# Kernel optimization log

Measured on AMD Instinct MI355X. Metric: run time of the kernel, lower is better.

The kernel has to match this reference:

```python
import jax, jax.numpy as jnp
import numpy as np

G_N, G_K, G_R = 1024, 32, 0.2
BN_EPS = 1e-5


def fps(p, n_sample):
    """Furthest point sampling. p: [B,N,3] -> idx [B,n_sample] int32."""
    B, N, _ = p.shape

    def step(carry, _):
        dist, last = carry  # dist [B,N], last [B]
        lp = jnp.take_along_axis(p, last[:, None, None], axis=1)  # [B,1,3]
        d = jnp.sum((p - lp) ** 2, axis=-1)  # [B,N]
        dist = jnp.minimum(dist, d)
        nxt = jnp.argmax(dist, axis=1).astype(jnp.int32)
        return (dist, nxt), last

    init = (jnp.full((B, N), 1e10, p.dtype), jnp.zeros((B,), jnp.int32))
    _, idx = jax.lax.scan(step, init, None, length=n_sample)
    return idx.T  # [B, n_sample]


def ball_query(p, q, k, r):
    """p: [B,N,3], q: [B,S,3] -> [B,S,k] int32 neighbor indices (pad with first)."""
    B, N, _ = p.shape
    sq = jnp.sum((q[:, :, None, :] - p[:, None, :, :]) ** 2, axis=-1)  # [B,S,N]
    idx = jnp.where(sq <= r * r, jnp.arange(N, dtype=jnp.int32)[None, None, :], N)
    idx = jnp.sort(idx, axis=-1)[..., :k]  # first k in-ball indices (by index order)
    first = idx[..., :1]
    return jnp.where(idx == N, first, idx).astype(jnp.int32)


def gather_group(x, idx):
    """x: [B,N,C], idx: [B,S,K] -> [B,S,K,C]."""
    B, S, K = idx.shape
    C = x.shape[-1]
    flat = jnp.take_along_axis(x, idx.reshape(B, S * K, 1), axis=1)
    return flat.reshape(B, S, K, C)


def mlp_bn_relu(x, W, b, gamma, beta):
    """1x1 conv + BatchNorm (batch stats) + ReLU on [B,S,K,Cin]."""
    x = jnp.einsum('bskc,cd->bskd', x, W) + b
    m = jnp.mean(x, axis=(0, 1, 2))
    v = jnp.var(x, axis=(0, 1, 2))
    x = (x - m) * jax.lax.rsqrt(v + BN_EPS) * gamma + beta
    return jax.nn.relu(x)


def setup_inputs() -> dict:
    key = jax.random.key(0)
    ks = jax.random.split(key, 8)
    B, N, C = 16, 4096, 64
    d_feats = [64, 64, 128]
    inp = {
        'f': jax.random.normal(ks[0], (B, N, C), dtype=jnp.float32),
        'p': jax.random.uniform(ks[1], (B, N, 3), dtype=jnp.float32),
    }
    d_in = C + 3
    for i, d_out in enumerate(d_feats):
        inp[f'W{i}'] = jax.random.normal(ks[2 + i], (d_in, d_out), dtype=jnp.float32) * 0.05
        inp[f'b{i}'] = jnp.zeros((d_out,), jnp.float32)
        inp[f'gamma{i}'] = jnp.ones((d_out,), jnp.float32)
        inp[f'beta{i}'] = jnp.zeros((d_out,), jnp.float32)
        d_in = d_out
    return inp


def reference(f, p, W0, b0, gamma0, beta0, W1, b1, gamma1, beta1, W2, b2, gamma2, beta2):
    qry_idx = fps(p, G_N)                                   # [B,S]
    qry_pnt = jnp.take_along_axis(p, qry_idx[..., None], axis=1)  # [B,S,3]
    grp_idx = ball_query(p, qry_pnt, G_K, G_R)              # [B,S,K]
    grp_pnt = gather_group(p, grp_idx) - qry_pnt[:, :, None, :]   # [B,S,K,3]
    grp_fea = jnp.concatenate([gather_group(f, grp_idx), grp_pnt], axis=-1)  # [B,S,K,C+3]
    x = mlp_bn_relu(grp_fea, W0, b0, gamma0, beta0)
    x = mlp_bn_relu(x, W1, b1, gamma1, beta1)
    x = mlp_bn_relu(x, W2, b2, gamma2, beta2)
    f_out = jnp.max(x, axis=2)  # max-pool over neighborhood -> [B,S,128]
    return (f_out, qry_pnt)
```

## Files before the change

kernel.cpp:

```cpp
#include <hip/hip_runtime.h>

#define NB 16
#define NP 4096
#define CF 64
#define NS 1024
#define NK 32
#define NROWS (NB*NS*NK)

typedef float f32x4 __attribute__((ext_vector_type(4)));
typedef __bf16 bf16x8 __attribute__((ext_vector_type(8)));
typedef unsigned short u16x8 __attribute__((ext_vector_type(8)));

__device__ __forceinline__ unsigned short f2bf(float f){
  unsigned u = __float_as_uint(f);
  return (unsigned short)((u + 0x7FFFu + ((u>>16)&1u)) >> 16);
}
__device__ __forceinline__ float bf2f(unsigned short s){
  return __uint_as_float(((unsigned)s)<<16);
}

__device__ __forceinline__ float dppmax_b1(float x){
  int y=__builtin_amdgcn_update_dpp(0,__float_as_int(x),0xB1,0xF,0xF,true);
  return fmaxf(x,__int_as_float(y));
}
__device__ __forceinline__ float dppmax_4e(float x){
  int y=__builtin_amdgcn_update_dpp(0,__float_as_int(x),0x4E,0xF,0xF,true);
  return fmaxf(x,__int_as_float(y));
}
__device__ __forceinline__ float dppmax_hm(float x){
  int y=__builtin_amdgcn_update_dpp(0,__float_as_int(x),0x141,0xF,0xF,true);
  return fmaxf(x,__int_as_float(y));
}
__device__ __forceinline__ float dppmax_m(float x){
  int y=__builtin_amdgcn_update_dpp(0,__float_as_int(x),0x140,0xF,0xF,true);
  return fmaxf(x,__int_as_float(y));
}

#define FPS_T 256
#define FPS_PT (NP/FPS_T)
__global__ __launch_bounds__(FPS_T) void fps_kernel(const float* __restrict__ p,
                                                    float* __restrict__ qry){
  __shared__ float4 P4[NP];
  __shared__ unsigned long long warr[2][4];
  const int b = blockIdx.x, tid = threadIdx.x;
  const int lane = tid & 63, wid = tid >> 6;
  const float* pb = p + (size_t)b*NP*3;
  float px[FPS_PT], py[FPS_PT], pz[FPS_PT], dist[FPS_PT];
#pragma unroll
  for (int g=0; g<4; g++){
    const int i0 = tid*FPS_PT + g*4;
    const float* src = pb + (size_t)i0*3;
    f32x4 a = *(const f32x4*)(src);
    f32x4 c = *(const f32x4*)(src+4);
    f32x4 d = *(const f32x4*)(src+8);
    px[g*4+0]=a[0]; py[g*4+0]=a[1]; pz[g*4+0]=a[2];
    px[g*4+1]=a[3]; py[g*4+1]=c[0]; pz[g*4+1]=c[1];
    px[g*4+2]=c[2]; py[g*4+2]=c[3]; pz[g*4+2]=d[0];
    px[g*4+3]=d[1]; py[g*4+3]=d[2]; pz[g*4+3]=d[3];
#pragma unroll
    for (int j=0;j<4;j++){
      P4[i0+j]=make_float4(px[g*4+j],py[g*4+j],pz[g*4+j],0.f);
      dist[g*4+j]=1e10f;
    }
  }
  __syncthreads();
  float4 lp0 = P4[0];
  float lx=lp0.x, ly=lp0.y, lz=lp0.z;
  for (int t=0;t<NS;t++){
    if (tid==0){
      size_t o=(size_t)(b*NS+t)*3;
      qry[o+0]=lx; qry[o+1]=ly; qry[o+2]=lz;
    }
    float bv=-1.0f; int bi=0;
#pragma unroll
    for (int j=0;j<FPS_PT;j++){
      float dx=__fsub_rn(px[j],lx), dy=__fsub_rn(py[j],ly), dz=__fsub_rn(pz[j],lz);
      float d=__fadd_rn(__fadd_rn(__fmul_rn(dx,dx),__fmul_rn(dy,dy)),__fmul_rn(dz,dz));
      dist[j]=fminf(dist[j],d);
      if (dist[j]>bv){ bv=dist[j]; bi=j; }
    }
    const int gbi = tid*FPS_PT + bi;
    float m = bv;
    m = dppmax_b1(m);
    m = dppmax_4e(m);
    m = dppmax_hm(m);
    m = dppmax_m(m);
    unsigned m0 = (unsigned)__builtin_amdgcn_readlane(__float_as_int(m), 0);
    unsigned m1 = (unsigned)__builtin_amdgcn_readlane(__float_as_int(m), 16);
    unsigned m2 = (unsigned)__builtin_amdgcn_readlane(__float_as_int(m), 32);
    unsigned m3 = (unsigned)__builtin_amdgcn_readlane(__float_as_int(m), 48);
    unsigned ma = m0>m1?m0:m1, mb = m2>m3?m2:m3;
    unsigned mu = ma>mb?ma:mb;
    unsigned long long ball = __ballot(__float_as_uint(bv)==mu);
    int srcl = (int)(__ffsll((long long)ball) - 1);
    int widx = __builtin_amdgcn_readlane(gbi, srcl);
    if (lane==0)
      warr[t&1][wid] = ((unsigned long long)mu<<32)
                     | (unsigned)(0xFFFFFFFFu-(unsigned)widx);
    __syncthreads();
    unsigned long long k0=warr[t&1][0], k1=warr[t&1][1],
                       k2=warr[t&1][2], k3=warr[t&1][3];
    unsigned long long ka = k0>k1?k0:k1, kb = k2>k3?k2:k3;
    unsigned long long bk = ka>kb?ka:kb;
    const int winner = (int)(0xFFFFFFFFu-(unsigned)(bk & 0xFFFFFFFFull));
    float4 lp = P4[winner];
    lx=lp.x; ly=lp.y; lz=lp.z;
  }
}

#define BQ_T 512
__global__ __launch_bounds__(BQ_T) void ballq_kernel(const float* __restrict__ p,
                                                     const float* __restrict__ qry,
                                                     int* __restrict__ grp){
  __shared__ float PX[NP], PY[NP], PZ[NP];
  const int tid = threadIdx.x, lane = tid & 63, w = tid >> 6;
  const int b  = blockIdx.x >> 7;
  const int s0 = (blockIdx.x & 127) * 8;
  const float* pb = p + (size_t)b*NP*3;
  for (int i = tid; i < NP; i += BQ_T){
    PX[i]=pb[i*3+0]; PY[i]=pb[i*3+1]; PZ[i]=pb[i*3+2];
  }
  __syncthreads();
  const int s = s0 + w;
  const float* q = qry + (size_t)(b*NS+s)*3;
  const float qx=q[0], qy=q[1], qz=q[2];
  int* out = grp + (size_t)(b*NS+s)*NK;
  const float RR = (float)(0.2*0.2);
  int cum = 0, first = 0;
  for (int j=0;j<NP/64;j++){
    const int idx = j*64 + lane;
    float dx=__fsub_rn(qx,PX[idx]), dy=__fsub_rn(qy,PY[idx]), dz=__fsub_rn(qz,PZ[idx]);
    float sq=__fadd_rn(__fadd_rn(__fmul_rn(dx,dx),__fmul_rn(dy,dy)),__fmul_rn(dz,dz));
    const bool in_r = (sq <= RR);
    unsigned long long ball = __ballot(in_r);
    if (ball){
      if (cum == 0) first = j*64 + (int)__builtin_ctzll(ball);
      int below = __builtin_amdgcn_mbcnt_hi((unsigned)(ball>>32),
                    __builtin_amdgcn_mbcnt_lo((unsigned)ball, 0));
      int pos = cum + below;
      if (in_r && pos < NK) out[pos] = idx;
      cum += (int)__popcll(ball);
      if (cum >= NK) break;
    }
  }
  const int cnt = cum < NK ? cum : NK;
  if (lane >= cnt && lane < NK) out[lane] = first;
}

__global__ void zero_slots_kernel(float* __restrict__ slots){
  int i = blockIdx.x*256 + threadIdx.x;
  if (i < 64*256) slots[i]=0.0f;
}

#define TPW 8
__global__ __launch_bounds__(256) void gemm0_kernel(const float* __restrict__ f,
    const float* __restrict__ p, const float* __restrict__ qry,
    const int* __restrict__ grp, const float* __restrict__ W0,
    const float* __restrict__ b0, unsigned short* __restrict__ ybuf,
    float* __restrict__ slots){
  const int tid=threadIdx.x, lane=tid&63, w=tid>>6;
  const int lg=lane>>4, lr=lane&15;
  bf16x8 bw[3][4];
#pragma unroll
  for (int kc=0;kc<3;kc++)
#pragma unroll
    for (int nt=0;nt<4;nt++){
      u16x8 t;
#pragma unroll
      for (int j=0;j<8;j++){
        int k = kc*32 + lg*8 + j, n = nt*16 + lr;
        float v = (k<67) ? W0[k*64+n] : 0.0f;
        t[j]=f2bf(v);
      }
      bw[kc][nt]=__builtin_bit_cast(bf16x8,t);
    }
  float bs[4];
#pragma unroll
  for (int nt=0;nt<4;nt++) bs[nt]=b0[nt*16+lr];
  float ssum[4]={0,0,0,0}, ssq[4]={0,0,0,0};
  const int base_row = blockIdx.x*512;
  const int b = base_row / (NS*NK);
  for (int ti=0;ti<TPW;ti++){
    const int R0 = base_row + (w*TPW+ti)*16;
    const int Ra = R0 + lr;
    const int idxp = grp[Ra];
    const float* frow = f + ((size_t)(b*NP+idxp))*64;
    f32x4 u0=*(const f32x4*)(frow + lg*8);
    f32x4 u1=*(const f32x4*)(frow + lg*8 + 4);
    f32x4 u2=*(const f32x4*)(frow + 32 + lg*8);
    f32x4 u3=*(const f32x4*)(frow + 36 + lg*8);
    u16x8 t0, t1;
#pragma unroll
    for (int j=0;j<4;j++){
      t0[j]=f2bf(u0[j]); t0[4+j]=f2bf(u1[j]);
      t1[j]=f2bf(u2[j]); t1[4+j]=f2bf(u3[j]);
    }
    u16x8 t2={0,0,0,0,0,0,0,0};
    if (lg==0){
      const int qidx = Ra >> 5;
      const float* pp = p + ((size_t)(b*NP+idxp))*3;
      const float* qq = qry + (size_t)qidx*3;
      t2[0]=f2bf(__fsub_rn(pp[0],qq[0]));
      t2[1]=f2bf(__fsub_rn(pp[1],qq[1]));
      t2[2]=f2bf(__fsub_rn(pp[2],qq[2]));
    }
    bf16x8 a0=__builtin_bit_cast(bf16x8,t0);
    bf16x8 a1=__builtin_bit_cast(bf16x8,t1);
    bf16x8 a2=__builtin_bit_cast(bf16x8,t2);
#pragma unroll
    for (int nt=0;nt<4;nt++){
      f32x4 acc={0,0,0,0};
      acc=__builtin_amdgcn_mfma_f32_16x16x32_bf16(a0,bw[0][nt],acc,0,0,0);
      acc=__builtin_amdgcn_mfma_f32_16x16x32_bf16(a1,bw[1][nt],acc,0,0,0);
      acc=__builtin_amdgcn_mfma_f32_16x16x32_bf16(a2,bw[2][nt],acc,0,0,0);
#pragma unroll
      for (int r=0;r<4;r++){
        float v = acc[r] + bs[nt];
        ssum[nt]+=v; ssq[nt]+=v*v;
        ybuf[(size_t)(R0 + lg*4 + r)*64 + nt*16 + lr] = f2bf(v);
      }
    }
  }
  float* slot = slots + (size_t)(blockIdx.x & 63)*256;
#pragma unroll
  for (int nt=0;nt<4;nt++){
    float s1=ssum[nt], s2=ssq[nt];
    s1 += __shfl_xor(s1,16); s1 += __shfl_xor(s1,32);
    s2 += __shfl_xor(s2,16); s2 += __shfl_xor(s2,32);
    if (lane<16){
      atomicAdd(slot + nt*16+lr, s1);
      atomicAdd(slot + 128 + nt*16+lr, s2);
    }
  }
}

__global__ void finalize_kernel(float* __restrict__ slots,
                                const float* __restrict__ gamma,
                                const float* __restrict__ beta,
                                float* __restrict__ par, int Cc){
  const int c = threadIdx.x;
  float s1=0.f, s2=0.f;
  for (int i=0;i<64;i++){ s1+=slots[i*256+c]; s2+=slots[i*256+128+c]; }
  const float invM = 1.0f/(float)NROWS;
  if (c<Cc){
    float mean = s1*invM;
    float var  = s2*invM - mean*mean;
    float scale = gamma[c]/sqrtf(var + 1e-5f);
    par[c]      = scale;
    par[128+c]  = beta[c] - mean*scale;
  }
  for (int i=0;i<64;i++){ slots[i*256+c]=0.f; slots[i*256+128+c]=0.f; }
}

__global__ __launch_bounds__(256) void gemm1_kernel(unsigned short* __restrict__ ybuf,
    const float* __restrict__ W, const float* __restrict__ bv,
    const float* __restrict__ par0, float* __restrict__ slots){
  const int tid=threadIdx.x, lane=tid&63, w=tid>>6;
  const int lg=lane>>4, lr=lane&15;
  float sc[2][8], sh[2][8];
#pragma unroll
  for (int kc=0;kc<2;kc++){
    int c0=kc*32+lg*8;
#pragma unroll
    for (int j=0;j<8;j++){ sc[kc][j]=par0[c0+j]; sh[kc][j]=par0[128+c0+j]; }
  }
  bf16x8 bw[2][4];
#pragma unroll
  for (int kc=0;kc<2;kc++)
#pragma unroll
    for (int nt=0;nt<4;nt++){
      u16x8 t;
#pragma unroll
      for (int j=0;j<8;j++){
        int k=kc*32+lg*8+j, n=nt*16+lr;
        t[j]=f2bf(W[k*64+n]);
      }
      bw[kc][nt]=__builtin_bit_cast(bf16x8,t);
    }
  float bs[4];
#pragma unroll
  for (int nt=0;nt<4;nt++) bs[nt]=bv[nt*16+lr];
  float ssum[4]={0,0,0,0}, ssq[4]={0,0,0,0};
  const int base_row = blockIdx.x*512;
  for (int ti=0;ti<TPW;ti++){
    const int R0 = base_row + (w*TPW+ti)*16;
    const unsigned short* yr = ybuf + (size_t)(R0+lr)*64;
    bf16x8 a[2];
#pragma unroll
    for (int kc=0;kc<2;kc++){
      u16x8 rv = *(const u16x8*)(yr + kc*32 + lg*8);
      u16x8 t;
#pragma unroll
      for (int j=0;j<8;j++){
        float v = bf2f(rv[j]);
        v = fmaxf(fmaf(v, sc[kc][j], sh[kc][j]), 0.f);
        t[j]=f2bf(v);
      }
      a[kc]=__builtin_bit_cast(bf16x8,t);
    }
#pragma unroll
    for (int nt=0;nt<4;nt++){
      f32x4 acc={0,0,0,0};
      acc=__builtin_amdgcn_mfma_f32_16x16x32_bf16(a[0],bw[0][nt],acc,0,0,0);
      acc=__builtin_amdgcn_mfma_f32_16x16x32_bf16(a[1],bw[1][nt],acc,0,0,0);
#pragma unroll
      for (int r=0;r<4;r++){
        float v = acc[r] + bs[nt];
        ssum[nt]+=v; ssq[nt]+=v*v;
        ybuf[(size_t)(R0 + lg*4 + r)*64 + nt*16 + lr] = f2bf(v);
      }
    }
  }
  float* slot = slots + (size_t)(blockIdx.x & 63)*256;
#pragma unroll
  for (int nt=0;nt<4;nt++){
    float s1=ssum[nt], s2=ssq[nt];
    s1 += __shfl_xor(s1,16); s1 += __shfl_xor(s1,32);
    s2 += __shfl_xor(s2,16); s2 += __shfl_xor(s2,32);
    if (lane<16){
      atomicAdd(slot + nt*16+lr, s1);
      atomicAdd(slot + 128 + nt*16+lr, s2);
    }
  }
}

__global__ __launch_bounds__(256) void gemm2stats_kernel(const unsigned short* __restrict__ ybuf,
    const float* __restrict__ W, const float* __restrict__ bv,
    const float* __restrict__ par1, float* __restrict__ slots){
  const int tid=threadIdx.x, lane=tid&63, w=tid>>6;
  const int lg=lane>>4, lr=lane&15;
  float sc[2][8], sh[2][8];
#pragma unroll
  for (int kc=0;kc<2;kc++){
    int c0=kc*32+lg*8;
#pragma unroll
    for (int j=0;j<8;j++){ sc[kc][j]=par1[c0+j]; sh[kc][j]=par1[128+c0+j]; }
  }
  bf16x8 bw[2][8];
#pragma unroll
  for (int kc=0;kc<2;kc++)
#pragma unroll
    for (int nt=0;nt<8;nt++){
      u16x8 t;
#pragma unroll
      for (int j=0;j<8;j++){
        int k=kc*32+lg*8+j, n=nt*16+lr;
        t[j]=f2bf(W[k*128+n]);
      }
      bw[kc][nt]=__builtin_bit_cast(bf16x8,t);
    }
  float bs[8], ssum[8], ssq[8];
#pragma unroll
  for (int nt=0;nt<8;nt++){ bs[nt]=bv[nt*16+lr]; ssum[nt]=0.f; ssq[nt]=0.f; }
  const int base_row = blockIdx.x*512;
  for (int ti=0;ti<TPW;ti++){
    const int R0 = base_row + (w*TPW+ti)*16;
    const unsigned short* yr = ybuf + (size_t)(R0+lr)*64;
    bf16x8 a[2];
#pragma unroll
    for (int kc=0;kc<2;kc++){
      u16x8 rv = *(const u16x8*)(yr + kc*32 + lg*8);
      u16x8 t;
#pragma unroll
      for (int j=0;j<8;j++){
        float v = bf2f(rv[j]);
        v = fmaxf(fmaf(v, sc[kc][j], sh[kc][j]), 0.f);
        t[j]=f2bf(v);
      }
      a[kc]=__builtin_bit_cast(bf16x8,t);
    }
#pragma unroll
    for (int nt=0;nt<8;nt++){
      f32x4 acc={0,0,0,0};
      acc=__builtin_amdgcn_mfma_f32_16x16x32_bf16(a[0],bw[0][nt],acc,0,0,0);
      acc=__builtin_amdgcn_mfma_f32_16x16x32_bf16(a[1],bw[1][nt],acc,0,0,0);
#pragma unroll
      for (int r=0;r<4;r++){
        float v = acc[r] + bs[nt];
        ssum[nt]+=v; ssq[nt]+=v*v;
      }
    }
  }
  float* slot = slots + (size_t)(blockIdx.x & 63)*256;
#pragma unroll
  for (int nt=0;nt<8;nt++){
    float s1=ssum[nt], s2=ssq[nt];
    s1 += __shfl_xor(s1,16); s1 += __shfl_xor(s1,32);
    s2 += __shfl_xor(s2,16); s2 += __shfl_xor(s2,32);
    if (lane<16){
      atomicAdd(slot + nt*16+lr, s1);
      atomicAdd(slot + 128 + nt*16+lr, s2);
    }
  }
}

#define QPW 8
__global__ __launch_bounds__(256) void gemm2max_kernel(const unsigned short* __restrict__ ybuf,
    const float* __restrict__ W, const float* __restrict__ bv,
    const float* __restrict__ par1, const float* __restrict__ par2,
    float* __restrict__ fout){
  const int tid=threadIdx.x, lane=tid&63, w=tid>>6;
  const int lg=lane>>4, lr=lane&15;
  float sc1[2][8], sh1[2][8];
#pragma unroll
  for (int kc=0;kc<2;kc++){
    int c0=kc*32+lg*8;
#pragma unroll
    for (int j=0;j<8;j++){ sc1[kc][j]=par1[c0+j]; sh1[kc][j]=par1[128+c0+j]; }
  }
  float sc2[8], sh2[8], bs[8];
#pragma unroll
  for (int nt=0;nt<8;nt++){
    int n=nt*16+lr;
    sc2[nt]=par2[n]; sh2[nt]=par2[128+n]; bs[nt]=bv[n];
  }
  bf16x8 bw[2][8];
#pragma unroll
  for (int kc=0;kc<2;kc++)
#pragma unroll
    for (int nt=0;nt<8;nt++){
      u16x8 t;
#pragma unroll
      for (int j=0;j<8;j++){
        int k=kc*32+lg*8+j, n=nt*16+lr;
        t[j]=f2bf(W[k*128+n]);
      }
      bw[kc][nt]=__builtin_bit_cast(bf16x8,t);
    }
  const int qbase = blockIdx.x*(4*QPW) + w*QPW;
  for (int qi=0;qi<QPW;qi++){
    const int gq = qbase + qi;
    float qmax[8];
#pragma unroll
    for (int nt=0;nt<8;nt++) qmax[nt]=-1e30f;
#pragma unroll
    for (int half=0; half<2; half++){
      const int R0 = gq*32 + half*16;
      const unsigned short* yr = ybuf + (size_t)(R0+lr)*64;
      bf16x8 a[2];
#pragma unroll
      for (int kc=0;kc<2;kc++){
        u16x8 rv = *(const u16x8*)(yr + kc*32 + lg*8);
        u16x8 t;
#pragma unroll
        for (int j=0;j<8;j++){
          float v = bf2f(rv[j]);
          v = fmaxf(fmaf(v, sc1[kc][j], sh1[kc][j]), 0.f);
          t[j]=f2bf(v);
        }
        a[kc]=__builtin_bit_cast(bf16x8,t);
      }
#pragma unroll
      for (int nt=0;nt<8;nt++){
        f32x4 acc={0,0,0,0};
        acc=__builtin_amdgcn_mfma_f32_16x16x32_bf16(a[0],bw[0][nt],acc,0,0,0);
        acc=__builtin_amdgcn_mfma_f32_16x16x32_bf16(a[1],bw[1][nt],acc,0,0,0);
        float m=-1e30f;
#pragma unroll
        for (int r=0;r<4;r++){
          float v = acc[r] + bs[nt];
          v = fmaxf(fmaf(v, sc2[nt], sh2[nt]), 0.f);
          m = fmaxf(m, v);
        }
        m = fmaxf(m, __shfl_xor(m,16));
        m = fmaxf(m, __shfl_xor(m,32));
        qmax[nt] = fmaxf(qmax[nt], m);
      }
    }
    if (lane<16){
#pragma unroll
      for (int nt=0;nt<8;nt++)
        fout[(size_t)gq*128 + nt*16 + lane] = qmax[nt];
    }
  }
}

extern "C" void kernel_launch(void* const* d_in, const int* in_sizes, int n_in,
                              void* d_out, int out_size, void* d_ws, size_t ws_size,
                              hipStream_t stream){
  const float* f   = (const float*)d_in[0];
  const float* p   = (const float*)d_in[1];
  const float* W0  = (const float*)d_in[2];
  const float* b0  = (const float*)d_in[3];
  const float* g0  = (const float*)d_in[4];
  const float* be0 = (const float*)d_in[5];
  const float* W1  = (const float*)d_in[6];
  const float* b1  = (const float*)d_in[7];
  const float* g1  = (const float*)d_in[8];
  const float* be1 = (const float*)d_in[9];
  const float* W2  = (const float*)d_in[10];
  const float* b2  = (const float*)d_in[11];
  const float* g2  = (const float*)d_in[12];
  const float* be2 = (const float*)d_in[13];

  float* out = (float*)d_out;
  float* qry = out + (size_t)NB*NS*128;

  char* w = (char*)d_ws;
  int* grp = (int*)w;
  unsigned short* ybuf = (unsigned short*)(w + (size_t)2*1024*1024);
  float* slots = (float*)(w + (size_t)2*1024*1024 + (size_t)NROWS*64*2);
  float* par0 = slots + 64*256;
  float* par1 = par0 + 256;
  float* par2 = par1 + 256;

  fps_kernel<<<NB, FPS_T, 0, stream>>>(p, qry);
  ballq_kernel<<<NB*(NS/8), BQ_T, 0, stream>>>(p, qry, grp);
  zero_slots_kernel<<<64, 256, 0, stream>>>(slots);
  gemm0_kernel<<<NROWS/512, 256, 0, stream>>>(f, p, qry, grp, W0, b0, ybuf, slots);
  finalize_kernel<<<1, 128, 0, stream>>>(slots, g0, be0, par0, 64);
  gemm1_kernel<<<NROWS/512, 256, 0, stream>>>(ybuf, W1, b1, par0, slots);
  finalize_kernel<<<1, 128, 0, stream>>>(slots, g1, be1, par1, 64);
  gemm2stats_kernel<<<NROWS/512, 256, 0, stream>>>(ybuf, W2, b2, par1, slots);
  finalize_kernel<<<1, 128, 0, stream>>>(slots, g2, be2, par2, 128);
  gemm2max_kernel<<<NB*NS/(4*QPW), 256, 0, stream>>>(ybuf, W2, b2, par1, par2, out);
}
```

Baseline: 731.3 us.

## Carry winner coordinates through FPS reduction and widen block to 512 threads

The FPS kernel now has each thread track the coordinates of its local furthest point instead of its index, and passes them through readlane and an 8-entry shared exchange. This removes the shared point array and the dependent LDS lookup of the winning point on the serial critical path. The block size doubles to 512, which halves the per-thread point count but adds a fourth, larger cross-wave reduction stage. Tie-breaking changes: the old code picked the lowest global index on equal distances, while the new cross-wave select prefers the lower wave only through strict comparison. That preference may not match the reference order in every tie case.

```diff
diff --git a/kernel.cpp b/kernel.cpp
--- a/kernel.cpp
+++ b/kernel.cpp
@@ -36,18 +36,21 @@
   return fmaxf(x,__int_as_float(y));
 }
 
-#define FPS_T 256
+__device__ __forceinline__ float4 sel4(bool c, float4 a, float4 b){
+  return make_float4(c?a.x:b.x, c?a.y:b.y, c?a.z:b.z, c?a.w:b.w);
+}
+
+#define FPS_T 512
 #define FPS_PT (NP/FPS_T)
 __global__ __launch_bounds__(FPS_T) void fps_kernel(const float* __restrict__ p,
                                                     float* __restrict__ qry){
-  __shared__ float4 P4[NP];
-  __shared__ unsigned long long warr[2][4];
+  __shared__ float4 ebuf[2][8];
   const int b = blockIdx.x, tid = threadIdx.x;
   const int lane = tid & 63, wid = tid >> 6;
   const float* pb = p + (size_t)b*NP*3;
   float px[FPS_PT], py[FPS_PT], pz[FPS_PT], dist[FPS_PT];
 #pragma unroll
-  for (int g=0; g<4; g++){
+  for (int g=0; g<2; g++){
     const int i0 = tid*FPS_PT + g*4;
     const float* src = pb + (size_t)i0*3;
     f32x4 a = *(const f32x4*)(src);
@@ -58,28 +61,22 @@
     px[g*4+2]=c[2]; py[g*4+2]=c[3]; pz[g*4+2]=d[0];
     px[g*4+3]=d[1]; py[g*4+3]=d[2]; pz[g*4+3]=d[3];
 #pragma unroll
-    for (int j=0;j<4;j++){
-      P4[i0+j]=make_float4(px[g*4+j],py[g*4+j],pz[g*4+j],0.f);
-      dist[g*4+j]=1e10f;
-    }
-  }
-  __syncthreads();
-  float4 lp0 = P4[0];
-  float lx=lp0.x, ly=lp0.y, lz=lp0.z;
+    for (int j=0;j<4;j++) dist[g*4+j]=1e10f;
+  }
+  float lx=pb[0], ly=pb[1], lz=pb[2];
   for (int t=0;t<NS;t++){
     if (tid==0){
       size_t o=(size_t)(b*NS+t)*3;
       qry[o+0]=lx; qry[o+1]=ly; qry[o+2]=lz;
     }
-    float bv=-1.0f; int bi=0;
+    float bv=-1.0f, wx=0.f, wy=0.f, wz=0.f;
 #pragma unroll
     for (int j=0;j<FPS_PT;j++){
       float dx=__fsub_rn(px[j],lx), dy=__fsub_rn(py[j],ly), dz=__fsub_rn(pz[j],lz);
       float d=__fadd_rn(__fadd_rn(__fmul_rn(dx,dx),__fmul_rn(dy,dy)),__fmul_rn(dz,dz));
       dist[j]=fminf(dist[j],d);
-      if (dist[j]>bv){ bv=dist[j]; bi=j; }
-    }
-    const int gbi = tid*FPS_PT + bi;
+      if (dist[j]>bv){ bv=dist[j]; wx=px[j]; wy=py[j]; wz=pz[j]; }
+    }
     float m = bv;
     m = dppmax_b1(m);
     m = dppmax_4e(m);
@@ -93,18 +90,21 @@
     unsigned mu = ma>mb?ma:mb;
     unsigned long long ball = __ballot(__float_as_uint(bv)==mu);
     int srcl = (int)(__ffsll((long long)ball) - 1);
-    int widx = __builtin_amdgcn_readlane(gbi, srcl);
-    if (lane==0)
-      warr[t&1][wid] = ((unsigned long long)mu<<32)
-                     | (unsigned)(0xFFFFFFFFu-(unsigned)widx);
+    float cx = __uint_as_float(__builtin_amdgcn_readlane(__float_as_int(wx), srcl));
+    float cy = __uint_as_float(__builtin_amdgcn_readlane(__float_as_int(wy), srcl));
+    float cz = __uint_as_float(__builtin_amdgcn_readlane(__float_as_int(wz), srcl));
+    if (lane==0) ebuf[t&1][wid] = make_float4(cx,cy,cz,__uint_as_float(mu));
     __syncthreads();
-    unsigned long long k0=warr[t&1][0], k1=warr[t&1][1],
-                       k2=warr[t&1][2], k3=warr[t&1][3];
-    unsigned long long ka = k0>k1?k0:k1, kb = k2>k3?k2:k3;
-    unsigned long long bk = ka>kb?ka:kb;
-    const int winner = (int)(0xFFFFFFFFu-(unsigned)(bk & 0xFFFFFFFFull));
-    float4 lp = P4[winner];
-    lx=lp.x; ly=lp.y; lz=lp.z;
+    float4 e0=ebuf[t&1][0], e1=ebuf[t&1][1], e2=ebuf[t&1][2], e3=ebuf[t&1][3];
+    float4 e4=ebuf[t&1][4], e5=ebuf[t&1][5], e6=ebuf[t&1][6], e7=ebuf[t&1][7];
+    float4 a01 = sel4(e1.w>e0.w, e1, e0);
+    float4 a23 = sel4(e3.w>e2.w, e3, e2);
+    float4 a45 = sel4(e5.w>e4.w, e5, e4);
+    float4 a67 = sel4(e7.w>e6.w, e7, e6);
+    float4 b03 = sel4(a23.w>a01.w, a23, a01);
+    float4 b47 = sel4(a67.w>a45.w, a67, a45);
+    float4 win = sel4(b47.w>b03.w, b47, b03);
+    lx=win.x; ly=win.y; lz=win.z;
   }
 }
 
```

Result: slower. 870.8 us (+19.1%).
